# Kernel tuning notes

Hardware: AMD Instinct MI355X
Metric: run time of the kernel (lower is better)

Reference implementation:

```python
import jax, jax.numpy as jnp
from jax import lax
import numpy as np
import math

B, H, W = 2, 48, 48
D_MODEL, D_STATE, D_CONV, EXPAND = 96, 16, 3, 2
D_INNER = EXPAND * D_MODEL
DT_RANK = math.ceil(D_MODEL / 16)
K = 6
L = H * W


def setup_inputs():
    key = jax.random.key(0)
    ks = jax.random.split(key, 10)
    x = jax.random.normal(ks[0], (B, H, W, D_MODEL), jnp.float32)
    y = jax.random.normal(ks[1], (B, H, W, D_MODEL), jnp.float32)
    k = jax.random.normal(ks[2], (B, H, W, D_MODEL), jnp.float32)
    in_proj_w = jax.random.normal(ks[3], (2 * D_INNER, D_MODEL), jnp.float32) * 0.02
    conv_w = jax.random.normal(ks[4], (D_INNER, 1, D_CONV, D_CONV), jnp.float32) * 0.1
    conv_b = jnp.zeros((D_INNER,), jnp.float32)
    x_proj_w = jax.random.normal(ks[5], (K, DT_RANK + 2 * D_STATE, D_INNER), jnp.float32) * 0.02
    s = DT_RANK ** -0.5
    dt_w = jax.random.uniform(ks[6], (K, D_INNER, DT_RANK), jnp.float32, -s, s)
    dt = jnp.exp(jax.random.uniform(ks[7], (K, D_INNER), jnp.float32)
                 * (math.log(0.1) - math.log(0.001)) + math.log(0.001))
    dt_b = dt + jnp.log(-jnp.expm1(-dt))  # inverse-softplus init as in dt_init
    A_logs = jnp.tile(jnp.log(jnp.arange(1, D_STATE + 1, dtype=jnp.float32))[None],
                      (K * D_INNER, 1))
    Ds = jnp.ones((K * D_INNER,), jnp.float32)
    ln_w = jnp.ones((D_INNER,), jnp.float32)
    ln_b = jnp.zeros((D_INNER,), jnp.float32)
    out_proj_w = jax.random.normal(ks[8], (D_MODEL, D_INNER), jnp.float32) * 0.02
    return dict(x=x, y=y, k=k, in_proj_w=in_proj_w, conv_w=conv_w, conv_b=conv_b,
                x_proj_w=x_proj_w, dt_w=dt_w, dt_b=dt_b, A_logs=A_logs, Ds=Ds,
                ln_w=ln_w, ln_b=ln_b, out_proj_w=out_proj_w)


def _diag_gather(t):
    # out[b,c,h,w] = t[b,c,h,(h+w)%W]; then (H,W)->(W,H) transpose, flatten
    idx = (jnp.arange(H)[:, None] + jnp.arange(W)[None, :]) % W
    g = jnp.take_along_axis(t, idx[None, None], axis=3)
    return jnp.swapaxes(g, -1, -2).reshape(t.shape[0], t.shape[1], L)


def _diag_scatter(flat):
    # inverse of _diag_gather: result[b,c,h,w] = r[b,c,h,(w-h)%W]
    r = jnp.swapaxes(flat.reshape(flat.shape[0], flat.shape[1], W, H), -1, -2)
    inv = (jnp.arange(W)[None, :] - jnp.arange(H)[:, None]) % W
    return jnp.take_along_axis(r, inv[None, None], axis=3)


def _forward(x, y, k, in_proj_w, conv_w, conv_b, x_proj_w, dt_w, dt_b,
             A_logs, Ds, ln_w, ln_b, out_proj_w):
    xv = jnp.einsum('bhwc,oc->bhwo', x, in_proj_w)[..., :D_INNER]
    yv = jnp.einsum('bhwc,oc->bhwo', y, in_proj_w)[..., :D_INNER]
    # NOTE: torch code overwrites z three times; the surviving gate z comes from k
    z = jnp.einsum('bhwc,oc->bhwo', k, in_proj_w)[..., D_INNER:]

    def conv_act(t):
        t = jnp.transpose(t, (0, 3, 1, 2))  # NCHW
        t = lax.conv_general_dilated(t, conv_w, (1, 1), ((1, 1), (1, 1)),
                                     feature_group_count=D_INNER,
                                     dimension_numbers=('NCHW', 'OIHW', 'NCHW'))
        return jax.nn.silu(t + conv_b[None, :, None, None])

    xc = conv_act(xv)  # (B,d,H,W)
    yc = conv_act(yv)

    h_x = xc.reshape(B, D_INNER, L)                                   # row-major
    v_y = jnp.swapaxes(yc, 2, 3).reshape(B, D_INNER, L)               # column-major
    diag_z = _diag_gather(yc)                                         # diagonal
    highfreq = jnp.stack([h_x, v_y, diag_z], axis=1)                  # (B,3,d,L)
    xs = jnp.concatenate([highfreq, jnp.flip(highfreq, axis=-1)], axis=1)  # (B,K,d,L)

    x_dbl = jnp.einsum('bkdl,kcd->bkcl', xs, x_proj_w)
    dts = jnp.einsum('bkrl,kdr->bkdl', x_dbl[:, :, :DT_RANK], dt_w)
    Bs = x_dbl[:, :, DT_RANK:DT_RANK + D_STATE]                       # (B,K,N,L)
    Cs = x_dbl[:, :, DT_RANK + D_STATE:]                              # (B,K,N,L)

    delta = jax.nn.softplus(dts + dt_b[None, :, :, None])             # (B,K,d,L)
    A = -jnp.exp(A_logs).reshape(K, D_INNER, D_STATE)
    Dk = Ds.reshape(K, D_INNER)

    def step(h, inp):
        dl, ul, Bl, Cl = inp  # (B,K,d),(B,K,d),(B,K,N),(B,K,N)
        h = jnp.exp(dl[..., None] * A) * h + (dl * ul)[..., None] * Bl[:, :, None, :]
        return h, jnp.einsum('bkdn,bkn->bkd', h, Cl)

    h0 = jnp.zeros((B, K, D_INNER, D_STATE), jnp.float32)
    seq = (jnp.moveaxis(delta, -1, 0), jnp.moveaxis(xs, -1, 0),
           jnp.moveaxis(Bs, -1, 0), jnp.moveaxis(Cs, -1, 0))
    _, ys = lax.scan(step, h0, seq)
    out_y = jnp.moveaxis(ys, 0, -1) + Dk[None, :, :, None] * xs       # (B,K,d,L)

    inv_y = jnp.flip(out_y[:, 3:6], axis=-1)

    def unT(t):  # undo the (W,H) raster used by vertical direction
        return jnp.swapaxes(t.reshape(B, D_INNER, W, H), -1, -2).reshape(B, D_INNER, L)

    y_h = out_y[:, 0] + inv_y[:, 0]
    y_v = unT(out_y[:, 1]) + unT(inv_y[:, 1])
    y_D = (_diag_scatter(out_y[:, 2]) + _diag_scatter(inv_y[:, 2])).reshape(B, D_INNER, L)

    zg = jax.nn.silu(z)

    def head(t):
        t = jnp.swapaxes(t, 1, 2).reshape(B, H, W, D_INNER)
        mu = t.mean(-1, keepdims=True)
        var = ((t - mu) ** 2).mean(-1, keepdims=True)
        t = (t - mu) * lax.rsqrt(var + 1e-5) * ln_w + ln_b
        return jnp.einsum('bhwd,od->bhwo', t * zg, out_proj_w)

    return head(y_h), head(y_v), head(y_D)


def reference(x, y, k, in_proj_w, conv_w, conv_b, x_proj_w, dt_w, dt_b,
              A_logs, Ds, ln_w, ln_b, out_proj_w):
    return _forward(x, y, k, in_proj_w, conv_w, conv_b, x_proj_w, dt_w, dt_b,
                    A_logs, Ds, ln_w, ln_b, out_proj_w)
```

## Files before the change

### kernel.cpp

```cpp
#include <hip/hip_runtime.h>
#include <hip/hip_bf16.h>

namespace {

constexpr int B_ = 2, H_ = 48, W_ = 48, DM_ = 96, DI_ = 192, NS_ = 16, RK_ = 6, K_ = 6;
constexpr int L_ = H_ * W_;
constexpr int C_ = 144;
constexpr int LC_ = L_ / C_;
constexpr int NPROJ = RK_ + 2 * NS_;
constexpr int NPAD = 48;

__device__ __forceinline__ float sigmoidf_(float x) { return 1.f / (1.f + __expf(-x)); }

__device__ __forceinline__ float delta_of(const float* __restrict__ dp,
                                          const float* __restrict__ wdt,
                                          float bias) {
  float s = bias;
#pragma unroll
  for (int r = 0; r < RK_; ++r) s += dp[r] * wdt[r];
  return (s > 20.f) ? s : __logf(1.f + __expf(s));
}

constexpr int IM = 32, IBK = 32;
__global__ void __launch_bounds__(256) k_inproj2(
    const float* __restrict__ x, const float* __restrict__ y,
    const float* __restrict__ kin, const float* __restrict__ inpw,
    float* __restrict__ xv, float* __restrict__ yv, float* __restrict__ zg) {
  __shared__ float As[IM][IBK + 1];
  __shared__ float Ws[IBK][DI_ + 1];
  int tid = threadIdx.x;
  constexpr int BPS = (B_ * L_) / IM;
  int s = blockIdx.x / BPS;
  int row0 = (blockIdx.x % BPS) * IM;
  const float* src = (s == 0) ? x : (s == 1) ? y : kin;
  float* dst = (s == 0) ? xv : (s == 1) ? yv : zg;
  int nbase = (s == 2) ? DI_ : 0;
  int tm = tid >> 4, tn = tid & 15;
  float acc[2][12];
#pragma unroll
  for (int i = 0; i < 2; ++i)
#pragma unroll
    for (int j = 0; j < 12; ++j) acc[i][j] = 0.f;

  for (int k0 = 0; k0 < DM_; k0 += IBK) {
    {
      int r = tid >> 3, c4 = (tid & 7) << 2;
      const float4 v = *reinterpret_cast<const float4*>(
          &src[(size_t)(row0 + r) * DM_ + k0 + c4]);
      As[r][c4] = v.x; As[r][c4 + 1] = v.y; As[r][c4 + 2] = v.z; As[r][c4 + 3] = v.w;
    }
#pragma unroll
    for (int it = 0; it < 6; ++it) {
      int i = tid + it * 256;
      int col = i >> 3, k4 = (i & 7) << 2;
      const float4 v = *reinterpret_cast<const float4*>(
          &inpw[(size_t)(nbase + col) * DM_ + k0 + k4]);
      Ws[k4 + 0][col] = v.x; Ws[k4 + 1][col] = v.y;
      Ws[k4 + 2][col] = v.z; Ws[k4 + 3][col] = v.w;
    }
    __syncthreads();
#pragma unroll
    for (int kk = 0; kk < IBK; ++kk) {
      float a0 = As[tm * 2 + 0][kk], a1 = As[tm * 2 + 1][kk];
      float w[12];
#pragma unroll
      for (int j = 0; j < 12; ++j) w[j] = Ws[kk][tn * 12 + j];
#pragma unroll
      for (int j = 0; j < 12; ++j) {
        acc[0][j] += a0 * w[j];
        acc[1][j] += a1 * w[j];
      }
    }
    __syncthreads();
  }
#pragma unroll
  for (int i = 0; i < 2; ++i) {
    size_t ob = (size_t)(row0 + tm * 2 + i) * DI_ + tn * 12;
#pragma unroll
    for (int j4 = 0; j4 < 3; ++j4) {
      float4 v;
      v.x = acc[i][j4 * 4 + 0]; v.y = acc[i][j4 * 4 + 1];
      v.z = acc[i][j4 * 4 + 2]; v.w = acc[i][j4 * 4 + 3];
      if (s == 2) {
        v.x *= sigmoidf_(v.x); v.y *= sigmoidf_(v.y);
        v.z *= sigmoidf_(v.z); v.w *= sigmoidf_(v.w);
      }
      *reinterpret_cast<float4*>(&dst[ob + j4 * 4]) = v;
    }
  }
}

__global__ void __launch_bounds__(192) k_conv_xs(
    const float* __restrict__ xv, const float* __restrict__ yv,
    const float* __restrict__ cw, const float* __restrict__ cb,
    float* __restrict__ xs) {
  __shared__ float scw[9 * DI_];
  int tid = threadIdx.x;
  for (int i = tid; i < 9 * DI_; i += 192) {
    int d = i / 9, j = i % 9;
    scw[j * DI_ + d] = cw[i];
  }
  __syncthreads();
  int p = tid / 48, q = tid % 48;
  int gl = blockIdx.x * 4 + p;
  int b = gl / L_, l = gl % L_;
  int h = l / W_, w = l % W_;
  int d4 = q << 2;
  float4 ax = *reinterpret_cast<const float4*>(&cb[d4]);
  float4 ay = ax;
#pragma unroll
  for (int kh = 0; kh < 3; ++kh) {
    int hh = h + kh - 1;
    if ((unsigned)hh >= (unsigned)H_) continue;
#pragma unroll
    for (int kw = 0; kw < 3; ++kw) {
      int ww = w + kw - 1;
      if ((unsigned)ww >= (unsigned)W_) continue;
      float4 wk = *reinterpret_cast<const float4*>(&scw[(kh * 3 + kw) * DI_ + d4]);
      size_t idx = ((size_t)b * L_ + hh * W_ + ww) * DI_ + d4;
      float4 vx = *reinterpret_cast<const float4*>(&xv[idx]);
      float4 vy = *reinterpret_cast<const float4*>(&yv[idx]);
      ax.x += vx.x * wk.x; ax.y += vx.y * wk.y; ax.z += vx.z * wk.z; ax.w += vx.w * wk.w;
      ay.x += vy.x * wk.x; ay.y += vy.y * wk.y; ay.z += vy.z * wk.z; ay.w += vy.w * wk.w;
    }
  }
  ax.x *= sigmoidf_(ax.x); ax.y *= sigmoidf_(ax.y);
  ax.z *= sigmoidf_(ax.z); ax.w *= sigmoidf_(ax.w);
  ay.x *= sigmoidf_(ay.x); ay.y *= sigmoidf_(ay.y);
  ay.z *= sigmoidf_(ay.z); ay.w *= sigmoidf_(ay.w);
  size_t base = (size_t)b * K_ * L_;
  int lv = w * H_ + h;
  int lv2 = ((w - h + W_) % W_) * H_ + h;
#define STORE6(kk, pos, val) \
  *reinterpret_cast<float4*>(&xs[(base + (size_t)(kk) * L_ + (pos)) * DI_ + d4]) = (val)
  STORE6(0, l, ax);
  STORE6(3, L_ - 1 - l, ax);
  STORE6(1, lv, ay);
  STORE6(4, L_ - 1 - lv, ay);
  STORE6(2, lv2, ay);
  STORE6(5, L_ - 1 - lv2, ay);
#undef STORE6
}

constexpr int XM = 32, XBK = 32;
__global__ void __launch_bounds__(256) k_xdbl3(
    const float* __restrict__ xs, const float* __restrict__ xpw,
    float* __restrict__ dts, float* __restrict__ Bsb, float* __restrict__ Csb) {
  __shared__ float As[XM][XBK + 1];
  __shared__ float Ws[XBK][NPAD];
  int tid = threadIdx.x;
  int row0 = blockIdx.x * XM;
  int k = (row0 / L_) % K_;
  int tm = tid >> 4, tn = tid & 15;
  for (int i = tid; i < XBK * (NPAD - NPROJ); i += 256) {
    int kk = i / (NPAD - NPROJ), c = NPROJ + i % (NPAD - NPROJ);
    Ws[kk][c] = 0.f;
  }
  float acc[2][3];
#pragma unroll
  for (int i = 0; i < 2; ++i)
#pragma unroll
    for (int j = 0; j < 3; ++j) acc[i][j] = 0.f;

  for (int k0 = 0; k0 < DI_; k0 += XBK) {
    {
      int r = tid >> 3, c4 = (tid & 7) << 2;
      const float4 v = *reinterpret_cast<const float4*>(
          &xs[(size_t)(row0 + r) * DI_ + k0 + c4]);
      As[r][c4] = v.x; As[r][c4 + 1] = v.y; As[r][c4 + 2] = v.z; As[r][c4 + 3] = v.w;
    }
#pragma unroll
    for (int it = 0; it < 2; ++it) {
      int i = tid + it * 256;
      if (i < NPROJ * 8) {
        int c = i >> 3, k4 = (i & 7) << 2;
        const float4 v = *reinterpret_cast<const float4*>(
            &xpw[((size_t)k * NPROJ + c) * DI_ + k0 + k4]);
        Ws[k4 + 0][c] = v.x; Ws[k4 + 1][c] = v.y;
        Ws[k4 + 2][c] = v.z; Ws[k4 + 3][c] = v.w;
      }
    }
    __syncthreads();
#pragma unroll
    for (int kk = 0; kk < XBK; ++kk) {
      float a0 = As[tm * 2 + 0][kk], a1 = As[tm * 2 + 1][kk];
      float w0 = Ws[kk][tn * 3 + 0], w1 = Ws[kk][tn * 3 + 1], w2 = Ws[kk][tn * 3 + 2];
      acc[0][0] += a0 * w0; acc[0][1] += a0 * w1; acc[0][2] += a0 * w2;
      acc[1][0] += a1 * w0; acc[1][1] += a1 * w1; acc[1][2] += a1 * w2;
    }
    __syncthreads();
  }
#pragma unroll
  for (int i = 0; i < 2; ++i) {
    int row = row0 + tm * 2 + i;
#pragma unroll
    for (int j = 0; j < 3; ++j) {
      int cc = tn * 3 + j;
      float v = acc[i][j];
      if (cc < RK_) dts[(size_t)row * RK_ + cc] = v;
      else if (cc < RK_ + NS_) Bsb[(size_t)row * NS_ + (cc - RK_)] = v;
      else if (cc < NPROJ) Csb[(size_t)row * NS_ + (cc - RK_ - NS_)] = v;
    }
  }
}

__global__ void __launch_bounds__(192) k_scan1(
    const float* __restrict__ dts, const float* __restrict__ dtw,
    const float* __restrict__ dtb, const float* __restrict__ xs,
    const float* __restrict__ Bsb, const float* __restrict__ A_logs,
    float* __restrict__ Sdl, float* __restrict__ SHin) {
  __shared__ float sB[LC_ * NS_];
  __shared__ float sdt[LC_ * RK_];
  int blk = blockIdx.x;
  int bk = blk / C_, c = blk % C_;
  int k = bk % K_;
  int d = threadIdx.x;
  size_t base = (size_t)bk * L_ + (size_t)c * LC_;
  for (int i = d; i < LC_ * NS_; i += 192) sB[i] = Bsb[base * NS_ + i];
  for (int i = d; i < LC_ * RK_; i += 192) sdt[i] = dts[base * RK_ + i];
  float A[NS_];
#pragma unroll
  for (int n = 0; n < NS_; ++n) A[n] = -__expf(A_logs[((size_t)k * DI_ + d) * NS_ + n]);
  float wdt[RK_];
#pragma unroll
  for (int r = 0; r < RK_; ++r) wdt[r] = dtw[((size_t)k * DI_ + d) * RK_ + r];
  float bias = dtb[k * DI_ + d];
  float S[NS_];
#pragma unroll
  for (int n = 0; n < NS_; ++n) S[n] = 0.f;
  float sum_dl = 0.f;
  __syncthreads();
  for (int l = 0; l < LC_; ++l) {
    float dl = delta_of(&sdt[l * RK_], wdt, bias);
    float u = xs[(base + l) * DI_ + d];
    float du = dl * u;
    sum_dl += dl;
    const float* Bp = &sB[l * NS_];
#pragma unroll
    for (int n = 0; n < NS_; ++n) {
      float e = __expf(dl * A[n]);
      S[n] = e * S[n] + du * Bp[n];
    }
  }
  Sdl[(size_t)blk * DI_ + d] = sum_dl;
  size_t ob = (size_t)blk * NS_ * DI_ + d;
#pragma unroll
  for (int n = 0; n < NS_; ++n) SHin[ob + (size_t)n * DI_] = S[n];
}

__global__ void __launch_bounds__(192) k_scan2(
    const float* __restrict__ Sdl, const float* __restrict__ A_logs,
    float* __restrict__ SHin) {
  int bkn = blockIdx.x;
  int bk = bkn / NS_, n = bkn % NS_;
  int k = bk % K_;
  int d = threadIdx.x;
  float A = -__expf(A_logs[((size_t)k * DI_ + d) * NS_ + n]);
  float h = 0.f;
  for (int c = 0; c < C_; ++c) {
    size_t i = ((size_t)(bk * C_ + c) * NS_ + n) * DI_ + d;
    float s = SHin[i];
    float p = __expf(A * Sdl[(size_t)(bk * C_ + c) * DI_ + d]);
    SHin[i] = h;
    h = p * h + s;
  }
}

__global__ void __launch_bounds__(192) k_scan3(
    const float* __restrict__ dts, const float* __restrict__ dtw,
    const float* __restrict__ dtb, const float* __restrict__ xs,
    const float* __restrict__ Bsb, const float* __restrict__ Csb,
    const float* __restrict__ A_logs, const float* __restrict__ Ds,
    const float* __restrict__ SHin, float* __restrict__ out_y) {
  __shared__ float sB[LC_ * NS_];
  __shared__ float sC[LC_ * NS_];
  __shared__ float sdt[LC_ * RK_];
  int blk = blockIdx.x;
  int bk = blk / C_, c = blk % C_;
  int k = bk % K_;
  int d = threadIdx.x;
  size_t base = (size_t)bk * L_ + (size_t)c * LC_;
  for (int i = d; i < LC_ * NS_; i += 192) {
    sB[i] = Bsb[base * NS_ + i];
    sC[i] = Csb[base * NS_ + i];
  }
  for (int i = d; i < LC_ * RK_; i += 192) sdt[i] = dts[base * RK_ + i];
  float A[NS_];
#pragma unroll
  for (int n = 0; n < NS_; ++n) A[n] = -__expf(A_logs[((size_t)k * DI_ + d) * NS_ + n]);
  float wdt[RK_];
#pragma unroll
  for (int r = 0; r < RK_; ++r) wdt[r] = dtw[((size_t)k * DI_ + d) * RK_ + r];
  float bias = dtb[k * DI_ + d];
  float Dk = Ds[k * DI_ + d];
  float h[NS_];
  size_t hb = (size_t)blk * NS_ * DI_ + d;
#pragma unroll
  for (int n = 0; n < NS_; ++n) h[n] = SHin[hb + (size_t)n * DI_];
  __syncthreads();
  for (int l = 0; l < LC_; ++l) {
    float dl = delta_of(&sdt[l * RK_], wdt, bias);
    float u = xs[(base + l) * DI_ + d];
    float du = dl * u;
    const float* Bp = &sB[l * NS_];
    const float* Cp = &sC[l * NS_];
    float yacc = 0.f;
#pragma unroll
    for (int n = 0; n < NS_; ++n) {
      h[n] = __expf(dl * A[n]) * h[n] + du * Bp[n];
      yacc += h[n] * Cp[n];
    }
    out_y[(base + l) * DI_ + d] = yacc + Dk * u;
  }
}

constexpr int MT = 32, GS_ = 196;
__global__ void __launch_bounds__(256) k_head2(
    const float* __restrict__ out_y, const float* __restrict__ zg,
    const float* __restrict__ lnw, const float* __restrict__ lnb,
    const float* __restrict__ opw, float* __restrict__ out) {
  __shared__ float Gs[MT][GS_];
  __shared__ float Ws[32][DM_ + 1];
  int tid = threadIdx.x;
  constexpr int BPS = (B_ * L_) / MT;
  int m = blockIdx.x / BPS;
  int r0 = (blockIdx.x % BPS) * MT;

  {
    int row = tid >> 3, t8 = tid & 7;
    int bl = r0 + row;
    int b = bl / L_, lp = bl % L_;
    int h = lp / W_, w = lp % W_;
    int l0;
    if (m == 0) l0 = lp;
    else if (m == 1) l0 = w * H_ + h;
    else l0 = ((w - h + W_) % W_) * H_ + h;
    size_t basef = ((size_t)b * K_ + m) * L_;
    size_t baser = ((size_t)b * K_ + m + 3) * L_;
    const float* pf = out_y + (basef + l0) * DI_;
    const float* pr = out_y + (baser + (size_t)(L_ - 1 - l0)) * DI_;
    float s = 0.f, s2 = 0.f;
#pragma unroll
    for (int j = 0; j < 6; ++j) {
      int c4 = t8 * 24 + j * 4;
      float4 a = *reinterpret_cast<const float4*>(&pf[c4]);
      float4 bb = *reinterpret_cast<const float4*>(&pr[c4]);
      float4 t;
      t.x = a.x + bb.x; t.y = a.y + bb.y; t.z = a.z + bb.z; t.w = a.w + bb.w;
      s += t.x + t.y + t.z + t.w;
      s2 += t.x * t.x + t.y * t.y + t.z * t.z + t.w * t.w;
      *reinterpret_cast<float4*>(&Gs[row][c4]) = t;
    }
    s += __shfl_xor(s, 1, 64);  s2 += __shfl_xor(s2, 1, 64);
    s += __shfl_xor(s, 2, 64);  s2 += __shfl_xor(s2, 2, 64);
    s += __shfl_xor(s, 4, 64);  s2 += __shfl_xor(s2, 4, 64);
    float mu = s * (1.f / DI_);
    float var = fmaxf(s2 * (1.f / DI_) - mu * mu, 0.f);
    float rs = rsqrtf(var + 1e-5f);
    const float* zp = zg + (size_t)bl * DI_;
#pragma unroll
    for (int j = 0; j < 6; ++j) {
      int c4 = t8 * 24 + j * 4;
      float4 t = *reinterpret_cast<const float4*>(&Gs[row][c4]);
      float4 zv = *reinterpret_cast<const float4*>(&zp[c4]);
      t.x = ((t.x - mu) * rs * lnw[c4 + 0] + lnb[c4 + 0]) * zv.x;
      t.y = ((t.y - mu) * rs * lnw[c4 + 1] + lnb[c4 + 1]) * zv.y;
      t.z = ((t.z - mu) * rs * lnw[c4 + 2] + lnb[c4 + 2]) * zv.z;
      t.w = ((t.w - mu) * rs * lnw[c4 + 3] + lnb[c4 + 3]) * zv.w;
      *reinterpret_cast<float4*>(&Gs[row][c4]) = t;
    }
  }
  __syncthreads();

  int tm = tid >> 4, tn = tid & 15;
  float acc[2][6];
#pragma unroll
  for (int i = 0; i < 2; ++i)
#pragma unroll
    for (int j = 0; j < 6; ++j) acc[i][j] = 0.f;

  for (int k0 = 0; k0 < DI_; k0 += 32) {
#pragma unroll
    for (int it = 0; it < 3; ++it) {
      int i = tid + it * 256;
      int o = i >> 3, k4 = (i & 7) << 2;
      const float4 v = *reinterpret_cast<const float4*>(
          &opw[(size_t)o * DI_ + k0 + k4]);
      Ws[k4 + 0][o] = v.x; Ws[k4 + 1][o] = v.y;
      Ws[k4 + 2][o] = v.z; Ws[k4 + 3][o] = v.w;
    }
    __syncthreads();
#pragma unroll
    for (int kk = 0; kk < 32; ++kk) {
      float a0 = Gs[tm * 2 + 0][k0 + kk], a1 = Gs[tm * 2 + 1][k0 + kk];
      float w[6];
#pragma unroll
      for (int j = 0; j < 6; ++j) w[j] = Ws[kk][tn * 6 + j];
#pragma unroll
      for (int j = 0; j < 6; ++j) {
        acc[0][j] += a0 * w[j];
        acc[1][j] += a1 * w[j];
      }
    }
    __syncthreads();
  }
  size_t obase = ((size_t)m * (B_ * L_) + r0) * DM_;
#pragma unroll
  for (int i = 0; i < 2; ++i) {
    size_t ob = obase + (size_t)(tm * 2 + i) * DM_ + tn * 6;
#pragma unroll
    for (int j = 0; j < 6; ++j) out[ob + j] = acc[i][j];
  }
}

}

extern "C" void kernel_launch(void* const* d_in, const int* in_sizes, int n_in,
                              void* d_out, int out_size, void* d_ws, size_t ws_size,
                              hipStream_t stream) {
  const float* x = (const float*)d_in[0];
  const float* y = (const float*)d_in[1];
  const float* kin = (const float*)d_in[2];
  const float* in_proj_w = (const float*)d_in[3];
  const float* conv_w = (const float*)d_in[4];
  const float* conv_b = (const float*)d_in[5];
  const float* x_proj_w = (const float*)d_in[6];
  const float* dt_w = (const float*)d_in[7];
  const float* dt_b = (const float*)d_in[8];
  const float* A_logs = (const float*)d_in[9];
  const float* Ds = (const float*)d_in[10];
  const float* ln_w = (const float*)d_in[11];
  const float* ln_b = (const float*)d_in[12];
  const float* out_proj_w = (const float*)d_in[13];
  float* out = (float*)d_out;

  float* ws = (float*)d_ws;
  const size_t BLD = (size_t)B_ * L_ * DI_;
  const size_t BKLD = (size_t)B_ * K_ * L_ * DI_;
  const size_t BKLN = (size_t)B_ * K_ * L_ * NS_;
  const size_t PSN = (size_t)B_ * K_ * C_ * NS_ * DI_;
  float* xv = ws;     ws += BLD;
  float* yv = ws;     ws += BLD;
  float* zg = ws;     ws += BLD;
  float* xs = ws;     ws += BKLD;
  float* Bsb = ws;    ws += BKLN;
  float* Csb = ws;    ws += BKLN;
  float* out_y = ws;  ws += BKLD;
  float* SHin = ws;   ws += PSN;
  float* Sdl = ws;    ws += (size_t)B_ * K_ * C_ * DI_;
  float* dts = ws;    ws += (size_t)B_ * K_ * L_ * RK_;

  k_inproj2<<<3 * B_ * L_ / IM, 256, 0, stream>>>(x, y, kin, in_proj_w, xv, yv, zg);
  k_conv_xs<<<B_ * L_ / 4, 192, 0, stream>>>(xv, yv, conv_w, conv_b, xs);
  k_xdbl3<<<B_ * K_ * L_ / XM, 256, 0, stream>>>(xs, x_proj_w, dts, Bsb, Csb);
  k_scan1<<<B_ * K_ * C_, 192, 0, stream>>>(dts, dt_w, dt_b, xs, Bsb, A_logs, Sdl, SHin);
  k_scan2<<<B_ * K_ * NS_, 192, 0, stream>>>(Sdl, A_logs, SHin);
  k_scan3<<<B_ * K_ * C_, 192, 0, stream>>>(dts, dt_w, dt_b, xs, Bsb, Csb, A_logs,
                                            Ds, SHin, out_y);
  k_head2<<<3 * B_ * L_ / MT, 256, 0, stream>>>(out_y, zg, ln_w, ln_b, out_proj_w, out);
}
```

Before: 162.6 us.

## Replace materialized 6-direction xs buffer with on-the-fly index remapping

Measured after the change: 161.3 us. About the same (-0.8%).

```diff
diff --git a/kernel.cpp b/kernel.cpp
--- a/kernel.cpp
+++ b/kernel.cpp
@@ -19,6 +19,15 @@
 #pragma unroll
   for (int r = 0; r < RK_; ++r) s += dp[r] * wdt[r];
   return (s > 20.f) ? s : __logf(1.f + __expf(s));
+}
+
+__device__ __forceinline__ int src_row(int k, int pos) {
+  int pk = (k >= 3) ? (L_ - 1 - pos) : pos;
+  int kk = (k >= 3) ? k - 3 : k;
+  if (kk == 0) return pk;
+  int h = pk % H_, wcol = pk / H_;
+  if (kk == 1) return h * W_ + wcol;
+  return h * W_ + (wcol + h) % W_;
 }
 
 constexpr int IM = 32, IBK = 32;
@@ -90,10 +99,10 @@
   }
 }
 
-__global__ void __launch_bounds__(192) k_conv_xs(
+__global__ void __launch_bounds__(192) k_conv2(
     const float* __restrict__ xv, const float* __restrict__ yv,
     const float* __restrict__ cw, const float* __restrict__ cb,
-    float* __restrict__ xs) {
+    float* __restrict__ xc, float* __restrict__ yc) {
   __shared__ float scw[9 * DI_];
   int tid = threadIdx.x;
   for (int i = tid; i < 9 * DI_; i += 192) {
@@ -128,29 +137,24 @@
   ax.z *= sigmoidf_(ax.z); ax.w *= sigmoidf_(ax.w);
   ay.x *= sigmoidf_(ay.x); ay.y *= sigmoidf_(ay.y);
   ay.z *= sigmoidf_(ay.z); ay.w *= sigmoidf_(ay.w);
-  size_t base = (size_t)b * K_ * L_;
-  int lv = w * H_ + h;
-  int lv2 = ((w - h + W_) % W_) * H_ + h;
-#define STORE6(kk, pos, val) \
-  *reinterpret_cast<float4*>(&xs[(base + (size_t)(kk) * L_ + (pos)) * DI_ + d4]) = (val)
-  STORE6(0, l, ax);
-  STORE6(3, L_ - 1 - l, ax);
-  STORE6(1, lv, ay);
-  STORE6(4, L_ - 1 - lv, ay);
-  STORE6(2, lv2, ay);
-  STORE6(5, L_ - 1 - lv2, ay);
-#undef STORE6
+  size_t ob = (size_t)gl * DI_ + d4;
+  *reinterpret_cast<float4*>(&xc[ob]) = ax;
+  *reinterpret_cast<float4*>(&yc[ob]) = ay;
 }
 
 constexpr int XM = 32, XBK = 32;
 __global__ void __launch_bounds__(256) k_xdbl3(
-    const float* __restrict__ xs, const float* __restrict__ xpw,
+    const float* __restrict__ xc, const float* __restrict__ yc,
+    const float* __restrict__ xpw,
     float* __restrict__ dts, float* __restrict__ Bsb, float* __restrict__ Csb) {
   __shared__ float As[XM][XBK + 1];
   __shared__ float Ws[XBK][NPAD];
   int tid = threadIdx.x;
   int row0 = blockIdx.x * XM;
+  int b = row0 / (K_ * L_);
   int k = (row0 / L_) % K_;
+  int pos0 = row0 % L_;
+  const float* usrc = ((k == 0 || k == 3) ? xc : yc) + (size_t)b * L_ * DI_;
   int tm = tid >> 4, tn = tid & 15;
   for (int i = tid; i < XBK * (NPAD - NPROJ); i += 256) {
     int kk = i / (NPAD - NPROJ), c = NPROJ + i % (NPAD - NPROJ);
@@ -165,8 +169,9 @@
   for (int k0 = 0; k0 < DI_; k0 += XBK) {
     {
       int r = tid >> 3, c4 = (tid & 7) << 2;
+      int srow = src_row(k, pos0 + r);
       const float4 v = *reinterpret_cast<const float4*>(
-          &xs[(size_t)(row0 + r) * DI_ + k0 + c4]);
+          &usrc[(size_t)srow * DI_ + k0 + c4]);
       As[r][c4] = v.x; As[r][c4 + 1] = v.y; As[r][c4 + 2] = v.z; As[r][c4 + 3] = v.w;
     }
 #pragma unroll
@@ -206,16 +211,19 @@
 
 __global__ void __launch_bounds__(192) k_scan1(
     const float* __restrict__ dts, const float* __restrict__ dtw,
-    const float* __restrict__ dtb, const float* __restrict__ xs,
-    const float* __restrict__ Bsb, const float* __restrict__ A_logs,
+    const float* __restrict__ dtb, const float* __restrict__ xc,
+    const float* __restrict__ yc, const float* __restrict__ Bsb,
+    const float* __restrict__ A_logs,
     float* __restrict__ Sdl, float* __restrict__ SHin) {
   __shared__ float sB[LC_ * NS_];
   __shared__ float sdt[LC_ * RK_];
   int blk = blockIdx.x;
   int bk = blk / C_, c = blk % C_;
-  int k = bk % K_;
+  int b = bk / K_, k = bk % K_;
   int d = threadIdx.x;
-  size_t base = (size_t)bk * L_ + (size_t)c * LC_;
+  const float* usrc = ((k == 0 || k == 3) ? xc : yc) + (size_t)b * L_ * DI_;
+  int pos0 = c * LC_;
+  size_t base = (size_t)bk * L_ + pos0;
   for (int i = d; i < LC_ * NS_; i += 192) sB[i] = Bsb[base * NS_ + i];
   for (int i = d; i < LC_ * RK_; i += 192) sdt[i] = dts[base * RK_ + i];
   float A[NS_];
@@ -232,7 +240,7 @@
   __syncthreads();
   for (int l = 0; l < LC_; ++l) {
     float dl = delta_of(&sdt[l * RK_], wdt, bias);
-    float u = xs[(base + l) * DI_ + d];
+    float u = usrc[(size_t)src_row(k, pos0 + l) * DI_ + d];
     float du = dl * u;
     sum_dl += dl;
     const float* Bp = &sB[l * NS_];
@@ -268,18 +276,21 @@
 
 __global__ void __launch_bounds__(192) k_scan3(
     const float* __restrict__ dts, const float* __restrict__ dtw,
-    const float* __restrict__ dtb, const float* __restrict__ xs,
-    const float* __restrict__ Bsb, const float* __restrict__ Csb,
-    const float* __restrict__ A_logs, const float* __restrict__ Ds,
-    const float* __restrict__ SHin, float* __restrict__ out_y) {
+    const float* __restrict__ dtb, const float* __restrict__ xc,
+    const float* __restrict__ yc, const float* __restrict__ Bsb,
+    const float* __restrict__ Csb, const float* __restrict__ A_logs,
+    const float* __restrict__ Ds, const float* __restrict__ SHin,
+    float* __restrict__ out_y) {
   __shared__ float sB[LC_ * NS_];
   __shared__ float sC[LC_ * NS_];
   __shared__ float sdt[LC_ * RK_];
   int blk = blockIdx.x;
   int bk = blk / C_, c = blk % C_;
-  int k = bk % K_;
+  int b = bk / K_, k = bk % K_;
   int d = threadIdx.x;
-  size_t base = (size_t)bk * L_ + (size_t)c * LC_;
+  const float* usrc = ((k == 0 || k == 3) ? xc : yc) + (size_t)b * L_ * DI_;
+  int pos0 = c * LC_;
+  size_t base = (size_t)bk * L_ + pos0;
   for (int i = d; i < LC_ * NS_; i += 192) {
     sB[i] = Bsb[base * NS_ + i];
     sC[i] = Csb[base * NS_ + i];
@@ -300,7 +311,7 @@
   __syncthreads();
   for (int l = 0; l < LC_; ++l) {
     float dl = delta_of(&sdt[l * RK_], wdt, bias);
-    float u = xs[(base + l) * DI_ + d];
+    float u = usrc[(size_t)src_row(k, pos0 + l) * DI_ + d];
     float du = dl * u;
     const float* Bp = &sB[l * NS_];
     const float* Cp = &sC[l * NS_];
@@ -442,7 +453,8 @@
   float* xv = ws;     ws += BLD;
   float* yv = ws;     ws += BLD;
   float* zg = ws;     ws += BLD;
-  float* xs = ws;     ws += BKLD;
+  float* xc = ws;     ws += BLD;
+  float* yc = ws;     ws += BLD;
   float* Bsb = ws;    ws += BKLN;
   float* Csb = ws;    ws += BKLN;
   float* out_y = ws;  ws += BKLD;
@@ -451,11 +463,12 @@
   float* dts = ws;    ws += (size_t)B_ * K_ * L_ * RK_;
 
   k_inproj2<<<3 * B_ * L_ / IM, 256, 0, stream>>>(x, y, kin, in_proj_w, xv, yv, zg);
-  k_conv_xs<<<B_ * L_ / 4, 192, 0, stream>>>(xv, yv, conv_w, conv_b, xs);
-  k_xdbl3<<<B_ * K_ * L_ / XM, 256, 0, stream>>>(xs, x_proj_w, dts, Bsb, Csb);
-  k_scan1<<<B_ * K_ * C_, 192, 0, stream>>>(dts, dt_w, dt_b, xs, Bsb, A_logs, Sdl, SHin);
+  k_conv2<<<B_ * L_ / 4, 192, 0, stream>>>(xv, yv, conv_w, conv_b, xc, yc);
+  k_xdbl3<<<B_ * K_ * L_ / XM, 256, 0, stream>>>(xc, yc, x_proj_w, dts, Bsb, Csb);
+  k_scan1<<<B_ * K_ * C_, 192, 0, stream>>>(dts, dt_w, dt_b, xc, yc, Bsb, A_logs,
+                                            Sdl, SHin);
   k_scan2<<<B_ * K_ * NS_, 192, 0, stream>>>(Sdl, A_logs, SHin);
-  k_scan3<<<B_ * K_ * C_, 192, 0, stream>>>(dts, dt_w, dt_b, xs, Bsb, Csb, A_logs,
-                                            Ds, SHin, out_y);
+  k_scan3<<<B_ * K_ * C_, 192, 0, stream>>>(dts, dt_w, dt_b, xc, yc, Bsb, Csb,
+                                            A_logs, Ds, SHin, out_y);
   k_head2<<<3 * B_ * L_ / MT, 256, 0, stream>>>(out_y, zg, ln_w, ln_b, out_proj_w, out);
 }
```
